# Kernel tuning notes

Hardware: AMD Instinct MI355X
Metric: run time of the kernel (lower is better)

The kernel has to match this reference:

```python
import jax, jax.numpy as jnp
import numpy as np

B, T, N = 16, 16, 1024          # patients, max visits, code_num
C, G, H, A, P = 48, 32, 150, 32, 32  # code_size, graph_size, hidden_size, t_attention_size, pool attn size
OUT = 1
NEG = -1e30


def setup_inputs() -> dict:
    key = jax.random.key(0)
    ks = jax.random.split(key, 20)
    code_x = (jax.random.uniform(ks[0], (B, T, N)) < 0.2).astype(jnp.float32)
    neighbors = (jax.random.uniform(ks[1], (B, T, N)) < 0.2).astype(jnp.float32)
    cat = jax.random.randint(ks[2], (B, T, N), 0, 8)
    # divided[..., 0/1/2] = disjoint m1 (persistent) / m2 (emerging-neighbor) / m3 (emerging-unrelated) masks
    divided = jnp.stack([(cat == 0), (cat == 1), (cat == 2)], axis=-1).astype(jnp.int32)
    lens = jax.random.randint(ks[3], (B,), 1, T + 1)
    prior = jax.random.uniform(ks[4], (N,))
    adj = (jax.random.uniform(ks[5], (N, N)) * (jax.random.uniform(ks[6], (N, N)) < 0.05)).astype(jnp.float32)

    def nrm(k, shape, scale=0.05):
        return (jax.random.normal(k, shape) * scale).astype(jnp.float32)

    return dict(
        code_x=code_x, divided=divided, neighbors=neighbors, lens=lens, prior=prior, adj=adj,
        c_emb=nrm(ks[7], (N, C)), n_emb=nrm(ks[8], (N, C)), u_emb=nrm(ks[9], (N, G)),
        Wg=nrm(ks[10], (C, G)), bg=jnp.zeros((G,), jnp.float32),
        W_ih=nrm(ks[11], (3 * H, G)), b_ih=jnp.zeros((3 * H,), jnp.float32),
        W_hh=nrm(ks[12], (3 * H, H)), b_hh=jnp.zeros((3 * H,), jnp.float32),
        Wq=nrm(ks[13], (G, A)), bq=jnp.zeros((A,), jnp.float32),
        Wk=nrm(ks[14], (G, A)), bk=jnp.zeros((A,), jnp.float32),
        Wv=nrm(ks[15], (G, H)), bv=jnp.zeros((H,), jnp.float32),
        Wp=nrm(ks[16], (H, P)), bp=jnp.zeros((P,), jnp.float32),
        ctx=nrm(ks[17], (P,)),
        Wc=nrm(ks[18], (H, OUT)), bc=jnp.zeros((OUT,), jnp.float32),
    )


def _forward(code_x, divided, neighbors, lens, prior, adj, c_emb, n_emb, u_emb,
             Wg, bg, W_ih, b_ih, W_hh, b_hh, Wq, bq, Wk, bk, Wv, bv,
             Wp, bp, ctx, Wc, bc):
    pr = prior[:, None]                                  # [N,1] disease prior scaling of graph messages
    scale = 1.0 / jnp.sqrt(jnp.asarray(A, jnp.float32))

    def gru(x, h):
        # torch nn.GRUCell semantics; x: [B,N,G], h: [B,N,H]
        gi = jnp.einsum('bng,kg->bnk', x, W_ih) + b_ih
        gh = jnp.einsum('bnh,kh->bnk', h, W_hh) + b_hh
        ir, iz, i_n = jnp.split(gi, 3, -1)
        hr, hz, h_n = jnp.split(gh, 3, -1)
        r = jax.nn.sigmoid(ir + hr)
        z = jax.nn.sigmoid(iz + hz)
        cand = jnp.tanh(i_n + r * h_n)
        return (1.0 - z) * cand + z * h

    def step(carry, xs):
        h_prev, no_prev, t = carry
        cx, nb, dv = xs                                  # [B,N], [B,N], [B,N,3]
        c = cx[..., None]
        n = nb[..., None]
        # --- GraphLayer: adjacency message passing, prior-weighted ---
        ce = c * c_emb                                   # [B,N,C]
        ne = n * n_emb
        agg_c = jnp.einsum('mn,bnc->bmc', adj, ce) * pr
        agg_n = jnp.einsum('mn,bnc->bmc', adj, ne) * pr
        co = jax.nn.leaky_relu((ce + c * (agg_c + agg_n)) @ Wg + bg)   # [B,N,G]
        no = jax.nn.leaky_relu((ne + n * (agg_n + agg_c)) @ Wg + bg)
        # --- TransitionLayer ---
        m1 = dv[..., 0] > 0
        m2 = dv[..., 1] > 0
        m3 = dv[..., 2] > 0
        m23 = m2 | m3
        h_gru = gru(co, h_prev)                          # GRU branch for persistent codes (m1)
        # attention branch: queries = prev-step neighbor embeddings (m2) or unrelated embeddings (m3)
        qf = jnp.where(m2[..., None], no_prev, 0.0) + jnp.where(m3[..., None], u_emb, 0.0)
        q = qf @ Wq + bq
        k = co @ Wk + bk
        v = co @ Wv + bv                                 # [B,N,H]
        g = jnp.einsum('bma,bna->bmn', q, k) * scale     # scores over active m2|m3 keys only
        g = jnp.where(m23[:, None, :], g, NEG)
        h_att = jnp.tanh(jnp.einsum('bmn,bnh->bmh', jax.nn.softmax(g, axis=-1), v))
        t_pos = (t > 0).astype(co.dtype)                 # m23 branch only runs for t > 0 (as in original)
        h_new = jnp.where(m1[..., None], h_gru, 0.0) + t_pos * jnp.where(m23[..., None], h_att, 0.0)
        # masked maxes (0 when the index set is empty, as in original)
        om1 = jnp.max(jnp.where(m1[..., None], h_gru, NEG), axis=1)
        om1 = jnp.where(jnp.any(m1, axis=1)[:, None], om1, 0.0)
        om23 = jnp.max(jnp.where(m23[..., None], h_att, NEG), axis=1)
        om23 = jnp.where(jnp.any(m23, axis=1)[:, None], om23, 0.0)
        out_t = om1 + t_pos * om23                       # [B,H]
        return (h_new, no, t + 1), out_t

    h0 = jnp.zeros((B, N, H), jnp.float32)
    no0 = jnp.zeros((B, N, G), jnp.float32)
    xs = (jnp.transpose(code_x, (1, 0, 2)),
          jnp.transpose(neighbors, (1, 0, 2)),
          jnp.transpose(divided, (1, 0, 2, 3)))
    _, outs = jax.lax.scan(step, (h0, no0, jnp.int32(0)), xs)
    outs = jnp.transpose(outs, (1, 0, 2))                # [B,T,H]
    # --- DotProductAttention pooling over valid (ragged) timesteps ---
    vu = (outs @ Wp + bp) @ ctx                          # [B,T]
    valid = jnp.arange(T)[None, :] < lens[:, None]
    score = jax.nn.softmax(jnp.where(valid, vu, NEG), axis=-1)
    pooled = jnp.sum(outs * score[..., None], axis=1)    # [B,H]
    # --- Classifier (dropout identity at eval, activation=None) ---
    return pooled @ Wc + bc


def reference(code_x, divided, neighbors, lens, prior, adj, c_emb, n_emb, u_emb,
              Wg, bg, W_ih, b_ih, W_hh, b_hh, Wq, bq, Wk, bk, Wv, bv,
              Wp, bp, ctx, Wc, bc):
    return _forward(code_x, divided, neighbors, lens, prior, adj, c_emb, n_emb, u_emb,
                    Wg, bg, W_ih, b_ih, W_hh, b_hh, Wq, bq, Wk, bk, Wv, bv,
                    Wp, bp, ctx, Wc, bc)
```

## Files before the change

### kernel.cpp

```cpp
#include <hip/hip_runtime.h>

#define B_ 16
#define T_ 16
#define N_ 1024
#define C_ 48
#define G_ 32
#define H_ 150
#define A_ 32
#define P_ 32
#define H3_ 450
#define NNZ_CAP 262144
#define CAP1 256
#define CAP23 384
#define CHCAP 40960
#define DCAP 256
#define SCALE_ 0.17677669529663687f

__device__ __forceinline__ unsigned fenc(float f){
  unsigned u = __float_as_uint(f);
  return (u & 0x80000000u) ? ~u : (u | 0x80000000u);
}
__device__ __forceinline__ float fdec(unsigned e){
  unsigned u = (e & 0x80000000u) ? (e & 0x7fffffffu) : ~e;
  return __uint_as_float(u);
}
__device__ __forceinline__ float sigmf(float x){ return 1.f/(1.f+__expf(-x)); }
__device__ __forceinline__ float wmaxf(float v){
  #pragma unroll
  for (int d=32; d>0; d>>=1) v = fmaxf(v, __shfl_xor(v,d));
  return v;
}

#define FMA16(W, PTR, ACC) do { \
    const float4* _c4 = (const float4*)(PTR); \
    float4 _c0=_c4[0], _c1=_c4[1], _c2=_c4[2], _c3=_c4[3]; \
    ACC[0]=fmaf((W),_c0.x,ACC[0]); ACC[1]=fmaf((W),_c0.y,ACC[1]); \
    ACC[2]=fmaf((W),_c0.z,ACC[2]); ACC[3]=fmaf((W),_c0.w,ACC[3]); \
    ACC[4]=fmaf((W),_c1.x,ACC[4]); ACC[5]=fmaf((W),_c1.y,ACC[5]); \
    ACC[6]=fmaf((W),_c1.z,ACC[6]); ACC[7]=fmaf((W),_c1.w,ACC[7]); \
    ACC[8]=fmaf((W),_c2.x,ACC[8]); ACC[9]=fmaf((W),_c2.y,ACC[9]); \
    ACC[10]=fmaf((W),_c2.z,ACC[10]); ACC[11]=fmaf((W),_c2.w,ACC[11]); \
    ACC[12]=fmaf((W),_c3.x,ACC[12]); ACC[13]=fmaf((W),_c3.y,ACC[13]); \
    ACC[14]=fmaf((W),_c3.z,ACC[14]); ACC[15]=fmaf((W),_c3.w,ACC[15]); \
  } while(0)

__global__ void k_csr_cnt(const float* __restrict__ adj, int* __restrict__ rcnt){
  int m = blockIdx.x; int tid = threadIdx.x;
  int c = 0;
  for (int n = tid; n < N_; n += 256) c += (adj[(size_t)m*N_+n] != 0.f) ? 1 : 0;
  __shared__ int sr[256];
  sr[tid]=c; __syncthreads();
  for (int s=128; s>0; s>>=1){ if (tid<s) sr[tid]+=sr[tid+s]; __syncthreads(); }
  if (tid==0) rcnt[m]=sr[0];
}
__global__ void k_csr_scan(const int* __restrict__ rcnt, int* __restrict__ rowptr){
  int lane = threadIdx.x;
  int s = 0;
  for (int r=0;r<16;++r) s += rcnt[lane*16+r];
  int incl = s;
  for (int d=1; d<64; d<<=1){ int y = __shfl_up(incl, d); if (lane>=d) incl += y; }
  int run = incl - s;
  for (int r=0;r<16;++r){ rowptr[lane*16+r] = run; run += rcnt[lane*16+r]; }
  if (lane==63) rowptr[N_] = incl;
}
__global__ void k_csr_fill(const float* __restrict__ adj, const float* __restrict__ prior,
                           const int* __restrict__ rowptr,
                           int* __restrict__ ccol, float* __restrict__ cval){
  int m = blockIdx.x; int lane = threadIdx.x;
  int base = rowptr[m];
  float pm = prior[m];
  for (int it=0; it<N_/64; ++it){
    int n = it*64+lane;
    float a = adj[(size_t)m*N_+n];
    bool pnz = (a != 0.f);
    unsigned long long mk = __ballot(pnz);
    if (pnz){
      int idx = base + __popcll(mk & ((1ULL<<lane)-1ULL));
      if (idx < NNZ_CAP){ ccol[idx]=n; cval[idx]=a*pm; }
    }
    base += __popcll(mk);
  }
}

__global__ void k_masks(const int* __restrict__ divided, int* __restrict__ lst23,
                        int* __restrict__ pos1,
                        int* __restrict__ cnt23, int* __restrict__ cnt1){
  int bt = blockIdx.x; int lane = threadIdx.x;
  int base23=0, base1=0;
  for (int it=0; it<N_/64; ++it){
    int n = it*64+lane;
    const int* dv = &divided[((size_t)bt*N_+n)*3];
    int d0=dv[0], d1=dv[1], d2=dv[2];
    bool p23 = (d1>0)||(d2>0); bool p1 = d0>0;
    unsigned long long mk23 = __ballot(p23);
    unsigned long long mk1  = __ballot(p1);
    unsigned long long ltm = (1ULL<<lane)-1ULL;
    if (p23){ int idx = base23 + __popcll(mk23 & ltm); lst23[(size_t)bt*N_+idx]=n; }
    if (p1){ int idx = base1 + __popcll(mk1 & ltm); pos1[(size_t)bt*N_+n]=idx; }
    base23 += __popcll(mk23); base1 += __popcll(mk1);
  }
  if (lane==0){ cnt23[bt]=base23; cnt1[bt]=base1; }
}

__global__ void k_chains(const int* __restrict__ divided,
                         unsigned* __restrict__ chN, int* __restrict__ nchN,
                         unsigned* __restrict__ chH, int* __restrict__ nchH,
                         unsigned* __restrict__ chLv, int* __restrict__ nLv,
                         unsigned* __restrict__ chD){
  int idx = blockIdx.x*256 + threadIdx.x;
  if (idx >= B_*N_) return;
  int b = idx >> 10, n = idx & (N_-1);
  unsigned m1m = 0;
  for (int t=0;t<T_;++t){
    int d0 = divided[(((size_t)(b*T_+t))*N_ + n)*3];
    if (d0>0) m1m |= (1u<<t);
  }
  unsigned heads = m1m & ~(m1m<<1);
  while (heads){
    int t0 = __builtin_ctz(heads); heads &= (heads-1u);
    unsigned run = m1m >> t0;
    int len = __builtin_ctz(~run);
    unsigned enc = ((unsigned)b<<18)|((unsigned)n<<8)|((unsigned)t0<<4)|(unsigned)(len-1);
    int f = 0;
    if (t0 >= 2){
      size_t pidx = ((size_t)(b*T_+t0-1)*N_ + n)*3;
      if ((divided[pidx+1] | divided[pidx+2]) > 0) f = 1;
    }
    if (f){ int i2 = atomicAdd(nchH,1); if (i2 < CHCAP) chH[i2]=enc; }
    else  { int i2 = atomicAdd(nchN,1); if (i2 < CHCAP) chN[i2]=enc; }
    if (len >= 2){ int i2 = atomicAdd(&nLv[1],1); if (i2 < 8192) chLv[i2]=enc; }
    if (len >= 3){ int i2 = atomicAdd(&nLv[2],1); if (i2 < 2048) chLv[8192+i2]=enc; }
    if (len >= 4){ int i2 = atomicAdd(&nLv[3],1); if (i2 < DCAP) chD[i2]=enc; }
  }
}

__global__ void k_wt(const float* __restrict__ W_ih, const float* __restrict__ W_hh,
                     const float* __restrict__ Wq, const float* __restrict__ bq,
                     const float* __restrict__ Wk, const float* __restrict__ Wv,
                     float* __restrict__ WihT, float* __restrict__ WhhT,
                     float* __restrict__ Md, float* __restrict__ WvT){
  int idx = blockIdx.x*256+threadIdx.x;
  if (idx < G_*H3_){ int g=idx/H3_, k=idx-g*H3_; WihT[g*H3_+k]=W_ih[(size_t)k*G_+g]; }
  int idx2 = idx - G_*H3_;
  if (idx2>=0 && idx2 < H_*H3_){ int h=idx2/H3_, k=idx2-h*H3_; WhhT[h*H3_+k]=W_hh[(size_t)k*H_+h]; }
  int e = idx - (G_*H3_ + H_*H3_);
  if (e>=0 && e<1024){
    int g=e>>5, gp=e&31;
    float acc=0.f;
    #pragma unroll
    for (int a=0;a<A_;++a) acc = fmaf(Wq[g*A_+a], Wk[gp*A_+a], acc);
    Md[e]=acc;
  }
  int e2 = e - 1024;
  if (e2>=0 && e2<32){
    float acc=0.f;
    #pragma unroll
    for (int a=0;a<A_;++a) acc = fmaf(Wk[e2*A_+a], bq[a], acc);
    Md[1024+e2]=acc;
  }
  int e3 = e - 1056;
  if (e3>=0 && e3 < H_*G_){
    int h = e3>>5, g = e3&31;
    WvT[e3] = Wv[(size_t)g*H_+h];
  }
}

__global__ void k_init(float* __restrict__ om23f, int* __restrict__ nchN,
                       int* __restrict__ nchH, int* __restrict__ nLv){
  int i = blockIdx.x*256+threadIdx.x;
  if (i<B_*T_*H_){ om23f[i]=0.f; }
  if (i==0){ *nchN = 0; *nchH = 0; }
  if (i<16) nLv[i]=0;
}

__global__ __launch_bounds__(256) void k_cono(
    const float* __restrict__ code_x, const float* __restrict__ neighbors,
    const int* __restrict__ divided,
    const int* __restrict__ rowptr, const int* __restrict__ ccol, const float* __restrict__ cval,
    const float* __restrict__ c_emb, const float* __restrict__ n_emb,
    const float* __restrict__ Wg, const float* __restrict__ bg,
    float* __restrict__ co, float* __restrict__ no_)
{
  __shared__ float sCo[4][C_], sNo[4][C_];
  int w = threadIdx.x >> 6, lane = threadIdx.x & 63;
  int gw = blockIdx.x*4 + w;
  int bt = gw >> 10, m = gw & (N_-1);
  int t = bt & (T_-1);
  const int* dv = &divided[(size_t)gw*3];
  int d0=dv[0], d1=dv[1], d2=dv[2];
  bool needCo = (d0|d1|d2) > 0;
  bool needNo = (t < T_-1) && (divided[((size_t)(gw+N_))*3+1] > 0);
  if (!needCo && !needNo) return;
  float cxm = code_x[gw], nbm = neighbors[gw];
  float acc = 0.f;
  bool needAcc = (needCo && cxm!=0.f) || (needNo && nbm!=0.f);
  if (needAcc){
    int s = rowptr[m], e = rowptr[m+1];
    if (s > NNZ_CAP) s = NNZ_CAP;
    if (e > NNZ_CAP) e = NNZ_CAP;
    int btN = bt << 10;
    for (int base = s; base < e; base += 64){
      int j = base + lane;
      int cc = 0; float wx = 0.f, wy = 0.f;
      if (j < e){
        cc = ccol[j];
        float cv = cval[j];
        float xs = code_x[btN+cc], ys = neighbors[btN+cc];
        wx = cv*xs; wy = cv*ys;
      }
      unsigned long long mk = __ballot(wx!=0.f || wy!=0.f);
      while (mk){
        int u0 = __builtin_ctzll(mk); mk &= (mk-1ULL);
        int u1 = -1;
        if (mk){ u1 = __builtin_ctzll(mk); mk &= (mk-1ULL); }
        int u1s = (u1>=0)? u1 : u0;
        int n0 = __shfl(cc,u0); float a0x=__shfl(wx,u0), a0y=__shfl(wy,u0);
        int n1 = __shfl(cc,u1s); float a1x=__shfl(wx,u1s), a1y=__shfl(wy,u1s);
        float ce0=0.f,ne0=0.f,ce1=0.f,ne1=0.f;
        if (lane < C_){
          ce0 = c_emb[(size_t)n0*C_+lane]; ne0 = n_emb[(size_t)n0*C_+lane];
          ce1 = c_emb[(size_t)n1*C_+lane]; ne1 = n_emb[(size_t)n1*C_+lane];
        }
        acc = fmaf(a0x, ce0, acc); acc = fmaf(a0y, ne0, acc);
        if (u1>=0){ acc = fmaf(a1x, ce1, acc); acc = fmaf(a1y, ne1, acc); }
      }
    }
  }
  if (lane < C_){
    sCo[w][lane] = cxm * (c_emb[(size_t)m*C_+lane] + acc);
    sNo[w][lane] = nbm * (n_emb[(size_t)m*C_+lane] + acc);
  }
  asm volatile("s_waitcnt lgkmcnt(0)" ::: "memory");
  int g = lane & 31; bool isNo = lane >= 32;
  const float* src = isNo ? sNo[w] : sCo[w];
  float a2 = bg[g];
  #pragma unroll
  for (int c=0;c<C_;++c) a2 = fmaf(src[c], Wg[c*G_+g], a2);
  float r = a2 >= 0.f ? a2 : 0.01f*a2;
  if (isNo ? needNo : needCo){
    float* dst = isNo ? no_ : co;
    dst[(size_t)gw*G_ + g] = r;
  }
}

__global__ __launch_bounds__(512) void k_attn(
    const float* __restrict__ co, const float* __restrict__ no_,
    const float* __restrict__ u_emb, const int* __restrict__ divided,
    const int* __restrict__ lst23, const int* __restrict__ cnt23, const int* __restrict__ pos1,
    const float* __restrict__ Md, const float* __restrict__ WvT, const float* __restrict__ bv,
    float* __restrict__ hsel, float* __restrict__ om23f)
{
  int b = blockIdx.x; int t = blockIdx.y + 1; int bt = b*T_ + t;
  int cnt = cnt23[bt]; if (cnt > CAP23) cnt = CAP23;
  if (cnt == 0) return;
  __shared__ int   sLst[CAP23];
  __shared__ __align__(16) float sCo[CAP23][G_];
  __shared__ float sL[CAP23];
  __shared__ unsigned sMax[H_];
  int tid = threadIdx.x;
  int grp = tid >> 8;
  int rr  = tid & 255;
  unsigned sent = fenc(-1e30f);
  for (int i=tid; i<cnt; i+=512) sLst[i] = lst23[(size_t)bt*N_+i];
  for (int i=tid; i<H_; i+=512) sMax[i] = sent;
  __syncthreads();
  for (int i=tid; i<cnt*8; i+=512){
    int rrow = i>>3, seg = i&7;
    float4 v = *(const float4*)&co[((((size_t)bt<<10) + sLst[rrow])<<5) + seg*4];
    *(float4*)&sCo[rrow][seg*4] = v;
  }
  int r0 = 2*rr, r1 = 2*rr+1;
  bool act0 = r0 < cnt, act1 = r1 < cnt;
  float qpp0[G_], qpp1[G_];
  {
    float4 qv0[8], qv1[8];
    if (act0){
      int n = sLst[r0];
      int d1 = divided[((size_t)bt*N_+n)*3+1];
      const float* qs = (d1>0) ? &no_[((((size_t)(bt-1))<<10)+n)<<5] : &u_emb[(size_t)n*G_];
      #pragma unroll
      for (int j=0;j<8;++j) qv0[j] = ((const float4*)qs)[j];
    } else {
      #pragma unroll
      for (int j=0;j<8;++j) qv0[j] = make_float4(0.f,0.f,0.f,0.f);
    }
    if (act1){
      int n = sLst[r1];
      int d1 = divided[((size_t)bt*N_+n)*3+1];
      const float* qs = (d1>0) ? &no_[((((size_t)(bt-1))<<10)+n)<<5] : &u_emb[(size_t)n*G_];
      #pragma unroll
      for (int j=0;j<8;++j) qv1[j] = ((const float4*)qs)[j];
    } else {
      #pragma unroll
      for (int j=0;j<8;++j) qv1[j] = make_float4(0.f,0.f,0.f,0.f);
    }
    #pragma unroll
    for (int j=0;j<G_;++j){ float dd = Md[1024+j]; qpp0[j]=dd; qpp1[j]=dd; }
    #pragma unroll
    for (int g=0; g<G_; ++g){
      float q0 = (g&3)==0 ? qv0[g>>2].x : (g&3)==1 ? qv0[g>>2].y : (g&3)==2 ? qv0[g>>2].z : qv0[g>>2].w;
      float q1 = (g&3)==0 ? qv1[g>>2].x : (g&3)==1 ? qv1[g>>2].y : (g&3)==2 ? qv1[g>>2].z : qv1[g>>2].w;
      const float4* mr = (const float4*)&Md[g*G_];
      #pragma unroll
      for (int j=0;j<8;++j){
        float4 mj = mr[j];
        qpp0[4*j+0]=fmaf(q0,mj.x,qpp0[4*j+0]); qpp1[4*j+0]=fmaf(q1,mj.x,qpp1[4*j+0]);
        qpp0[4*j+1]=fmaf(q0,mj.y,qpp0[4*j+1]); qpp1[4*j+1]=fmaf(q1,mj.y,qpp1[4*j+1]);
        qpp0[4*j+2]=fmaf(q0,mj.z,qpp0[4*j+2]); qpp1[4*j+2]=fmaf(q1,mj.z,qpp1[4*j+2]);
        qpp0[4*j+3]=fmaf(q0,mj.w,qpp0[4*j+3]); qpp1[4*j+3]=fmaf(q1,mj.w,qpp1[4*j+3]);
      }
    }
  }
  __syncthreads();
  int half = (cnt+1)>>1;
  int c0 = grp ? half : 0;
  int c1 = grp ? cnt  : half;
  float pb0[G_], pb1[G_]; float l0=0.f, l1=0.f;
  #pragma unroll
  for (int j=0;j<G_;++j){ pb0[j]=0.f; pb1[j]=0.f; }
  if (act0){
    for (int c=c0;c<c1;++c){
      const float4* col = (const float4*)&sCo[c][0];
      float4 xv[8];
      #pragma unroll
      for (int j=0;j<8;++j) xv[j]=col[j];
      float dA=0.f,dB=0.f,dC=0.f,dD=0.f, eA=0.f,eB=0.f,eC=0.f,eD=0.f;
      #pragma unroll
      for (int j=0;j<8;++j){
        dA = fmaf(qpp0[4*j+0], xv[j].x, dA); dB = fmaf(qpp0[4*j+1], xv[j].y, dB);
        dC = fmaf(qpp0[4*j+2], xv[j].z, dC); dD = fmaf(qpp0[4*j+3], xv[j].w, dD);
        eA = fmaf(qpp1[4*j+0], xv[j].x, eA); eB = fmaf(qpp1[4*j+1], xv[j].y, eB);
        eC = fmaf(qpp1[4*j+2], xv[j].z, eC); eD = fmaf(qpp1[4*j+3], xv[j].w, eD);
      }
      float pv0 = __expf(((dA+dB)+(dC+dD))*SCALE_);
      float pv1 = __expf(((eA+eB)+(eC+eD))*SCALE_);
      if (!act1) pv1 = 0.f;
      l0 += pv0; l1 += pv1;
      #pragma unroll
      for (int j=0;j<8;++j){
        pb0[4*j+0]=fmaf(pv0,xv[j].x,pb0[4*j+0]); pb1[4*j+0]=fmaf(pv1,xv[j].x,pb1[4*j+0]);
        pb0[4*j+1]=fmaf(pv0,xv[j].y,pb0[4*j+1]); pb1[4*j+1]=fmaf(pv1,xv[j].y,pb1[4*j+1]);
        pb0[4*j+2]=fmaf(pv0,xv[j].z,pb0[4*j+2]); pb1[4*j+2]=fmaf(pv1,xv[j].z,pb1[4*j+2]);
        pb0[4*j+3]=fmaf(pv0,xv[j].w,pb0[4*j+3]); pb1[4*j+3]=fmaf(pv1,xv[j].w,pb1[4*j+3]);
      }
    }
  }
  __syncthreads();
  if (grp==0){
    if (act0){
      #pragma unroll
      for (int j=0;j<G_;++j) sCo[r0][(j+r0)&31] = pb0[j];
      sL[r0] = l0;
    }
    if (act1){
      #pragma unroll
      for (int j=0;j<G_;++j) sCo[r1][(j+r1)&31] = pb1[j];
      sL[r1] = l1;
    }
  }
  __syncthreads();
  if (grp==1){
    if (act0){
      #pragma unroll
      for (int j=0;j<G_;++j) sCo[r0][(j+r0)&31] += pb0[j];
      sL[r0] += l0;
    }
    if (act1){
      #pragma unroll
      for (int j=0;j<G_;++j) sCo[r1][(j+r1)&31] += pb1[j];
      sL[r1] += l1;
    }
  }
  __syncthreads();
  int grp2 = tid >> 8;
  int lane = tid & 63;
  int hA = grp2*75, hB = hA + 75;
  for (int er = tid & 255; er < CAP23; er += 256){
    bool act = er < cnt;
    float pb[G_];
    if (act){
      float inv = 1.f / sL[er];
      #pragma unroll
      for (int j=0;j<G_;++j) pb[j] = sCo[er][(j+er)&31] * inv;
    } else {
      #pragma unroll
      for (int j=0;j<G_;++j) pb[j]=0.f;
    }
    bool wsel=false; float* hd=nullptr;
    if (act && t+1 < T_){
      int n = sLst[er];
      size_t nidx = ((size_t)b*T_+(t+1))*N_ + n;
      if (divided[nidx*3+0] > 0){
        int pos = pos1[nidx];
        if (pos >= 0 && pos < CAP1){ wsel=true; hd=&hsel[(((size_t)b*T_+t)*CAP1 + pos)*H_]; }
      }
    }
    for (int h=hA; h<hB; ++h){
      float acc = bv[h];
      const float4* wr = (const float4*)&WvT[h*G_];
      #pragma unroll
      for (int j=0;j<8;++j){
        float4 wj = wr[j];
        acc = fmaf(pb[4*j+0], wj.x, acc);
        acc = fmaf(pb[4*j+1], wj.y, acc);
        acc = fmaf(pb[4*j+2], wj.z, acc);
        acc = fmaf(pb[4*j+3], wj.w, acc);
      }
      float o = act ? tanhf(acc) : -1e30f;
      float om = wmaxf(o);
      if (lane==0) atomicMax(&sMax[h], fenc(om));
      if (wsel) hd[h] = o;
    }
    if (cnt <= 256) break;
  }
  __syncthreads();
  for (int i=tid; i<H_; i+=512) om23f[(size_t)bt*H_+i] = fdec(sMax[i]);
}

__global__ __launch_bounds__(256) void k_gruheadN(
    const float* __restrict__ co, const int* __restrict__ pos1,
    const unsigned* __restrict__ chN, const int* __restrict__ nchN,
    const float* __restrict__ WihT, const float* __restrict__ b_ih,
    const float* __restrict__ b_hh, float* __restrict__ gout)
{
  __shared__ __align__(16) float sCoT[G_][16];
  __shared__ float sG[16][452];
  __shared__ int sBt[16], sN[16], sPos[16];
  int tid = threadIdx.x;
  int NC = *nchN; if (NC > CHCAP) NC = CHCAP;
  int base = blockIdx.x * 16;
  if (base >= NC) return;
  int num = min(16, NC - base);
  if (tid < 16){
    if (tid < num){
      unsigned cl = chN[base+tid];
      int b = cl>>18, n = (cl>>8)&1023, t0 = (cl>>4)&15;
      int bt = b*T_ + t0;
      sBt[tid]=bt; sN[tid]=n; sPos[tid]=pos1[(size_t)bt*N_+n];
    } else { sBt[tid]=0; sN[tid]=0; sPos[tid]=-1; }
  }
  __syncthreads();
  for (int i=tid; i<G_*16; i+=256){
    int g = i>>4, ii = i&15;
    sCoT[g][ii] = (ii<num) ? co[((size_t)sBt[ii]*N_+sN[ii])*G_+g] : 0.f;
  }
  __syncthreads();
  for (int pass=0; pass<2; ++pass){
    int k = pass*256 + tid;
    if (k < H3_){
      float acc[16];
      #pragma unroll
      for (int u=0;u<16;++u) acc[u]=0.f;
      for (int g=0; g<G_; ++g){
        float wih = WihT[g*H3_ + k];
        FMA16(wih, &sCoT[g][0], acc);
      }
      #pragma unroll
      for (int u=0;u<16;++u) sG[u][k] = acc[u];
    }
  }
  __syncthreads();
  for (int i=tid; i<num*152; i+=256){
    int s = i/152, h = i - s*152;
    if (h < H_){
      int pos = sPos[s];
      if (pos >= 0 && pos < CAP1){
        float r = sigmf(sG[s][h]       + b_ih[h]       + b_hh[h]);
        float z = sigmf(sG[s][h+H_]    + b_ih[h+H_]    + b_hh[h+H_]);
        float cand = tanhf(sG[s][h+2*H_] + b_ih[h+2*H_] + r*b_hh[h+2*H_]);
        gout[((size_t)sBt[s]*CAP1 + pos)*H_ + h] = (1.f-z)*cand;
      }
    }
  }
}

__global__ __launch_bounds__(256) void k_gruheadH(
    const float* __restrict__ co, const float* __restrict__ hsel,
    const int* __restrict__ pos1,
    const unsigned* __restrict__ chH, const int* __restrict__ nchH,
    const float* __restrict__ WihT, const float* __restrict__ b_ih,
    const float* __restrict__ WhhT, const float* __restrict__ b_hh,
    float* __restrict__ gout)
{
  __shared__ __align__(16) float sCoT[G_][16];
  __shared__ __align__(16) float sHT[152][16];
  __shared__ float sG[16][452];
  __shared__ float sGhn[16][152];
  __shared__ int sBt[16], sN[16], sPos[16], sHo[16];
  int tid = threadIdx.x;
  int NC = *nchH; if (NC > CHCAP) NC = CHCAP;
  int base = blockIdx.x * 16;
  if (base >= NC) return;
  int num = min(16, NC - base);
  if (tid < 16){
    if (tid < num){
      unsigned cl = chH[base+tid];
      int b = cl>>18, n = (cl>>8)&1023, t0 = (cl>>4)&15;
      int bt = b*T_ + t0;
      int pos = pos1[(size_t)bt*N_+n];
      sBt[tid]=bt; sN[tid]=n; sPos[tid]=pos;
      sHo[tid] = (b*T_ + (t0-1))*CAP1 + ((pos>=0 && pos<CAP1) ? pos : 0);
    } else { sBt[tid]=0; sN[tid]=0; sPos[tid]=-1; sHo[tid]=0; }
  }
  __syncthreads();
  for (int i=tid; i<G_*16; i+=256){
    int g = i>>4, ii = i&15;
    sCoT[g][ii] = (ii<num) ? co[((size_t)sBt[ii]*N_+sN[ii])*G_+g] : 0.f;
  }
  for (int i=tid; i<152*16; i+=256){
    int q = i>>4, ii = i&15;
    float v = 0.f;
    if (ii < num && q < H_) v = hsel[(size_t)sHo[ii]*H_ + q];
    sHT[q][ii] = v;
  }
  __syncthreads();
  for (int pass=0; pass<2; ++pass){
    int k = pass*256 + tid;
    if (k < H3_){
      float acc[16];
      #pragma unroll
      for (int u=0;u<16;++u) acc[u]=0.f;
      for (int g=0; g<G_; ++g){
        float wih = WihT[g*H3_ + k];
        FMA16(wih, &sCoT[g][0], acc);
      }
      #pragma unroll
      for (int u=0;u<16;++u) sG[u][k] = acc[u];
    }
  }
  for (int pass=0; pass<2; ++pass){
    int k = pass*256 + tid;
    if (k < H3_){
      float acc[16];
      #pragma unroll
      for (int u=0;u<16;++u) acc[u]=0.f;
      for (int q=0; q<H_; ++q){
        float whh = WhhT[q*H3_ + k];
        FMA16(whh, &sHT[q][0], acc);
      }
      if (k < 2*H_){
        #pragma unroll
        for (int u=0;u<16;++u) sG[u][k] += acc[u];
      } else {
        #pragma unroll
        for (int u=0;u<16;++u) sGhn[u][k-2*H_] = acc[u];
      }
    }
  }
  __syncthreads();
  for (int i=tid; i<num*152; i+=256){
    int s = i/152, h = i - s*152;
    if (h < H_){
      int pos = sPos[s];
      if (pos >= 0 && pos < CAP1){
        float hv = sHT[h][s];
        float r = sigmf(sG[s][h]       + b_ih[h]       + b_hh[h]);
        float z = sigmf(sG[s][h+H_]    + b_ih[h+H_]    + b_hh[h+H_]);
        float cand = tanhf(sG[s][h+2*H_] + b_ih[h+2*H_] + r*(sGhn[s][h] + b_hh[h+2*H_]));
        float o = (1.f-z)*cand + z*hv;
        gout[((size_t)sBt[s]*CAP1 + pos)*H_ + h] = o;
      }
    }
  }
}

__global__ __launch_bounds__(256) void k_grulev(
    const float* __restrict__ co, const int* __restrict__ pos1,
    const unsigned* __restrict__ chLv, const int* __restrict__ nLv,
    const float* __restrict__ WihT, const float* __restrict__ b_ih,
    const float* __restrict__ WhhT, const float* __restrict__ b_hh,
    float* __restrict__ gout, int s, int cap)
{
  __shared__ __align__(16) float sCoT[G_][16];
  __shared__ __align__(16) float sHT[152][16];
  __shared__ float sG[16][452];
  __shared__ float sGhn[16][152];
  __shared__ int sBt[16], sN[16], sPos[16], sHo[16];
  int tid = threadIdx.x;
  int NC = *nLv; if (NC > cap) NC = cap;
  int base = blockIdx.x * 16;
  if (base >= NC) return;
  int num = min(16, NC - base);
  if (tid < 16){
    if (tid < num){
      unsigned cl = chLv[base+tid];
      int b = cl>>18, n = (cl>>8)&1023, t0 = (cl>>4)&15;
      int bt = b*T_ + t0 + s;
      int pos = pos1[(size_t)bt*N_+n];
      int posp = pos1[(size_t)(bt-1)*N_+n];
      if (posp < 0 || posp >= CAP1) posp = 0;
      sBt[tid]=bt; sN[tid]=n; sPos[tid]=pos;
      sHo[tid] = (bt-1)*CAP1 + posp;
    } else { sBt[tid]=0; sN[tid]=0; sPos[tid]=-1; sHo[tid]=0; }
  }
  __syncthreads();
  for (int i=tid; i<G_*16; i+=256){
    int g = i>>4, ii = i&15;
    sCoT[g][ii] = (ii<num) ? co[((size_t)sBt[ii]*N_+sN[ii])*G_+g] : 0.f;
  }
  for (int i=tid; i<152*16; i+=256){
    int q = i>>4, ii = i&15;
    float v = 0.f;
    if (ii < num && q < H_) v = gout[(size_t)sHo[ii]*H_ + q];
    sHT[q][ii] = v;
  }
  __syncthreads();
  for (int pass=0; pass<2; ++pass){
    int k = pass*256 + tid;
    if (k < H3_){
      float acc[16];
      #pragma unroll
      for (int u=0;u<16;++u) acc[u]=0.f;
      for (int g=0; g<G_; ++g){
        float wih = WihT[g*H3_ + k];
        FMA16(wih, &sCoT[g][0], acc);
      }
      #pragma unroll
      for (int u=0;u<16;++u) sG[u][k] = acc[u];
    }
  }
  for (int pass=0; pass<2; ++pass){
    int k = pass*256 + tid;
    if (k < H3_){
      float acc[16];
      #pragma unroll
      for (int u=0;u<16;++u) acc[u]=0.f;
      for (int q=0; q<H_; ++q){
        float whh = WhhT[q*H3_ + k];
        FMA16(whh, &sHT[q][0], acc);
      }
      if (k < 2*H_){
        #pragma unroll
        for (int u=0;u<16;++u) sG[u][k] += acc[u];
      } else {
        #pragma unroll
        for (int u=0;u<16;++u) sGhn[u][k-2*H_] = acc[u];
      }
    }
  }
  __syncthreads();
  for (int i=tid; i<num*152; i+=256){
    int sl = i/152, h = i - sl*152;
    if (h < H_){
      int pos = sPos[sl];
      if (pos >= 0 && pos < CAP1){
        float hv = sHT[h][sl];
        float r = sigmf(sG[sl][h]       + b_ih[h]       + b_hh[h]);
        float z = sigmf(sG[sl][h+H_]    + b_ih[h+H_]    + b_hh[h+H_]);
        float cand = tanhf(sG[sl][h+2*H_] + b_ih[h+2*H_] + r*(sGhn[sl][h] + b_hh[h+2*H_]));
        float o = (1.f-z)*cand + z*hv;
        gout[((size_t)sBt[sl]*CAP1 + pos)*H_ + h] = o;
      }
    }
  }
}

__global__ __launch_bounds__(256) void k_grudeep(
    const float* __restrict__ co, const int* __restrict__ pos1,
    const unsigned* __restrict__ chD, const int* __restrict__ nD,
    const float* __restrict__ WihT, const float* __restrict__ b_ih,
    const float* __restrict__ WhhT, const float* __restrict__ b_hh,
    float* __restrict__ gout)
{
  __shared__ float hst[4][4][H_];
  int w = threadIdx.x >> 6, lane = threadIdx.x & 63;
  int NC = *nD; if (NC > DCAP) NC = DCAP;
  if (NC == 0) return;
  int cbase = (blockIdx.x*4 + w)*4;
  if (cbase >= NC) return;

  int cbv[4], cnv[4], t0v[4], lenv[4];
  #pragma unroll
  for (int u=0;u<4;++u){
    int cid = cbase+u; bool ca = cid < NC;
    unsigned cl = chD[ca ? cid : (NC-1)];
    cbv[u]=cl>>18; cnv[u]=(cl>>8)&1023; t0v[u]=(cl>>4)&15;
    lenv[u]= ca ? (int)((cl&15)+1) : 3;
  }
  int maxlen = lenv[0];
  #pragma unroll
  for (int u=1;u<4;++u) maxlen = max(maxlen, lenv[u]);

  int h0=lane,h1=lane+64,h2=lane+128; bool has2=(h2<H_); int h2c=has2?h2:0;
  float bi[9], bh[9];
  bi[0]=b_ih[h0]; bi[1]=b_ih[h0+H_]; bi[2]=b_ih[h0+2*H_];
  bi[3]=b_ih[h1]; bi[4]=b_ih[h1+H_]; bi[5]=b_ih[h1+2*H_];
  bi[6]=b_ih[h2c]; bi[7]=b_ih[h2c+H_]; bi[8]=b_ih[h2c+2*H_];
  bh[0]=b_hh[h0]; bh[1]=b_hh[h0+H_]; bh[2]=b_hh[h0+2*H_];
  bh[3]=b_hh[h1]; bh[4]=b_hh[h1+H_]; bh[5]=b_hh[h1+2*H_];
  bh[6]=b_hh[h2c]; bh[7]=b_hh[h2c+H_]; bh[8]=b_hh[h2c+2*H_];

  for (int s=3; s<maxlen; ++s){
    bool as[4]; int btv[4];
    const float* hp[4];
    #pragma unroll
    for (int u=0;u<4;++u){
      as[u] = s < lenv[u];
      int t = t0v[u] + (as[u] ? s : 0);
      btv[u] = cbv[u]*T_ + t;
      if (s == 3 && as[u]){
        int btp = btv[u] - 1;
        int posp = pos1[(size_t)btp*N_ + cnv[u]];
        if (posp < 0 || posp >= CAP1) posp = 0;
        hp[u] = &gout[((size_t)btp*CAP1 + posp)*H_];
      } else {
        hp[u] = &hst[w][u][0];
      }
    }
    float gi[4][9], gh[4][9];
    #pragma unroll
    for (int u=0;u<4;++u){
      #pragma unroll
      for (int j=0;j<9;++j){ gi[u][j]=bi[j]; gh[u][j]=bh[j]; }
    }
    const float* cop[4];
    #pragma unroll
    for (int u=0;u<4;++u) cop[u] = &co[((size_t)btv[u]*N_ + cnv[u])*G_];
    for (int g=0; g<G_; ++g){
      const float* wr = &WihT[g*H3_];
      float wv[9];
      wv[0]=wr[h0]; wv[1]=wr[h0+H_]; wv[2]=wr[h0+2*H_];
      wv[3]=wr[h1]; wv[4]=wr[h1+H_]; wv[5]=wr[h1+2*H_];
      wv[6]=wr[h2c]; wv[7]=wr[h2c+H_]; wv[8]=wr[h2c+2*H_];
      #pragma unroll
      for (int u=0;u<4;++u){
        float cg = cop[u][g];
        #pragma unroll
        for (int j=0;j<9;++j) gi[u][j]=fmaf(cg, wv[j], gi[u][j]);
      }
    }
    for (int q=0;q<H_;++q){
      const float* wr=&WhhT[q*H3_];
      float wv[9];
      wv[0]=wr[h0]; wv[1]=wr[h0+H_]; wv[2]=wr[h0+2*H_];
      wv[3]=wr[h1]; wv[4]=wr[h1+H_]; wv[5]=wr[h1+2*H_];
      wv[6]=wr[h2c]; wv[7]=wr[h2c+H_]; wv[8]=wr[h2c+2*H_];
      #pragma unroll
      for (int u=0;u<4;++u){
        float hv = hp[u][q];
        #pragma unroll
        for (int j=0;j<9;++j) gh[u][j]=fmaf(hv, wv[j], gh[u][j]);
      }
    }
    #pragma unroll
    for (int u=0;u<4;++u){
      if (as[u]){
        float hv0 = hp[u][h0];
        float hv1 = hp[u][h1];
        float hv2 = has2 ? hp[u][h2] : 0.f;
        float r0=sigmf(gi[u][0]+gh[u][0]), z0=sigmf(gi[u][1]+gh[u][1]);
        float cd0=tanhf(gi[u][2]+r0*gh[u][2]);
        float o0=(1.f-z0)*cd0 + z0*hv0;
        float r1=sigmf(gi[u][3]+gh[u][3]), z1=sigmf(gi[u][4]+gh[u][4]);
        float cd1=tanhf(gi[u][5]+r1*gh[u][5]);
        float o1=(1.f-z1)*cd1 + z1*hv1;
        float o2=0.f;
        if (has2){
          float r2=sigmf(gi[u][6]+gh[u][6]), z2=sigmf(gi[u][7]+gh[u][7]);
          float cd2=tanhf(gi[u][8]+r2*gh[u][8]);
          o2=(1.f-z2)*cd2 + z2*hv2;
        }
        float* hd = &hst[w][u][0];
        hd[h0]=o0; hd[h1]=o1; if (has2) hd[h2]=o2;
        int pos = pos1[(size_t)btv[u]*N_ + cnv[u]];
        if (pos >= 0 && pos < CAP1){
          float* gd = &gout[((size_t)btv[u]*CAP1 + pos)*H_];
          gd[h0]=o0; gd[h1]=o1; if (has2) gd[h2]=o2;
        }
      }
    }
    asm volatile("s_waitcnt lgkmcnt(0)" ::: "memory");
  }
}

__global__ __launch_bounds__(256) void k_om1(
    const float* __restrict__ gout, const int* __restrict__ cnt1, float* __restrict__ om1f)
{
  int bt = blockIdx.x; int tid = threadIdx.x;
  int c1 = cnt1[bt]; if (c1 > CAP1) c1 = CAP1;
  if (tid < H_){
    float mx = -1e30f;
    for (int r=0;r<c1;++r) mx = fmaxf(mx, gout[((size_t)bt*CAP1+r)*H_+tid]);
    om1f[(size_t)bt*H_+tid] = (c1>0) ? mx : 0.f;
  }
}

__global__ __launch_bounds__(256) void k_final(
    const float* __restrict__ om1f, const float* __restrict__ om23f,
    const float* __restrict__ Wp, const float* __restrict__ bp,
    const float* __restrict__ ctx, const float* __restrict__ Wc, const float* __restrict__ bc,
    const int* __restrict__ lens, float* __restrict__ out)
{
  int b = blockIdx.x; int tid = threadIdx.x;
  __shared__ float sOut[T_][H_];
  __shared__ float sTP[T_][P_];
  __shared__ float sVu[T_], sSc[T_], sPool[H_];
  __shared__ float sRed[256];
  for (int i=tid; i<T_*H_; i+=256){
    int t=i/H_, h=i-t*H_;
    float o1 = om1f[((size_t)b*T_+t)*H_+h];
    float o2 = (t>0)? om23f[((size_t)b*T_+t)*H_+h] : 0.f;
    sOut[t][h]=o1+o2;
  }
  __syncthreads();
  for (int pr = tid; pr < T_*P_; pr += 256){
    int t = pr / P_, p = pr - t*P_;
    float acc = bp[p];
    for (int h=0;h<H_;++h) acc = fmaf(sOut[t][h], Wp[h*P_+p], acc);
    sTP[t][p] = acc * ctx[p];
  }
  __syncthreads();
  if (tid < T_){
    float v=0.f;
    for (int p=0;p<P_;++p) v += sTP[tid][p];
    sVu[tid]=v;
  }
  __syncthreads();
  if (tid==0){
    int L = lens[b]; if (L<1) L=1; if (L>T_) L=T_;
    float mx=-1e30f;
    for (int t=0;t<L;++t) mx = fmaxf(mx, sVu[t]);
    float s=0.f;
    for (int t=0;t<L;++t){ float e=__expf(sVu[t]-mx); sSc[t]=e; s+=e; }
    float inv=1.f/s;
    for (int t=0;t<T_;++t) sSc[t] = (t<L)? sSc[t]*inv : 0.f;
  }
  __syncthreads();
  if (tid < H_){
    float acc=0.f;
    for (int t=0;t<T_;++t) acc = fmaf(sOut[t][tid], sSc[t], acc);
    sPool[tid]=acc;
  }
  __syncthreads();
  float v = (tid<H_)? sPool[tid]*Wc[tid] : 0.f;
  sRed[tid]=v; __syncthreads();
  for (int s=128;s>0;s>>=1){ if (tid<s) sRed[tid]+=sRed[tid+s]; __syncthreads(); }
  if (tid==0) out[b] = sRed[0] + bc[0];
}

extern "C" void kernel_launch(void* const* d_in, const int* in_sizes, int n_in,
                              void* d_out, int out_size, void* d_ws, size_t ws_size,
                              hipStream_t stream)
{
  const float* code_x=(const float*)d_in[0];
  const int*   divided=(const int*)d_in[1];
  const float* neighbors=(const float*)d_in[2];
  const int*   lens=(const int*)d_in[3];
  const float* prior=(const float*)d_in[4];
  const float* adj=(const float*)d_in[5];
  const float* c_emb=(const float*)d_in[6];
  const float* n_emb=(const float*)d_in[7];
  const float* u_emb=(const float*)d_in[8];
  const float* Wg=(const float*)d_in[9];
  const float* bg=(const float*)d_in[10];
  const float* W_ih=(const float*)d_in[11];
  const float* b_ih=(const float*)d_in[12];
  const float* W_hh=(const float*)d_in[13];
  const float* b_hh=(const float*)d_in[14];
  const float* Wq=(const float*)d_in[15];
  const float* bq=(const float*)d_in[16];
  const float* Wk=(const float*)d_in[17];
  const float* bk=(const float*)d_in[18];
  const float* Wv=(const float*)d_in[19];
  const float* bv=(const float*)d_in[20];
  const float* Wp=(const float*)d_in[21];
  const float* bp=(const float*)d_in[22];
  const float* ctx=(const float*)d_in[23];
  const float* Wc=(const float*)d_in[24];
  const float* bc=(const float*)d_in[25];
  float* out=(float*)d_out;
  (void)in_sizes; (void)n_in; (void)out_size; (void)ws_size; (void)bk;

  char* p=(char*)d_ws;
  size_t off=0;
  auto carve=[&](size_t bytes)->char*{ char* r=p+off; off=(off+bytes+255)&~(size_t)255; return r; };
  int*   rowptr=(int*)carve((N_+1)*4);
  int*   rcnt  =(int*)carve(N_*4);
  int*   ccol  =(int*)carve((size_t)NNZ_CAP*4);
  float* cval  =(float*)carve((size_t)NNZ_CAP*4);
  int*   cnt23 =(int*)carve(B_*T_*4);
  int*   cnt1  =(int*)carve(B_*T_*4);
  int*   lst23 =(int*)carve((size_t)B_*T_*N_*4);
  int*   pos1  =(int*)carve((size_t)B_*T_*N_*4);
  float* co    =(float*)carve((size_t)B_*T_*N_*G_*4);
  float* no_   =(float*)carve((size_t)B_*T_*N_*G_*4);
  float* WihT  =(float*)carve((size_t)G_*H3_*4);
  float* WhhT  =(float*)carve((size_t)H_*H3_*4);
  float* Md    =(float*)carve(1056*4);
  float* WvT   =(float*)carve((size_t)H_*G_*4);
  float* hsel  =(float*)carve((size_t)B_*T_*CAP1*H_*4);
  float* gout  =(float*)carve((size_t)B_*T_*CAP1*H_*4);
  unsigned* chainsN=(unsigned*)carve((size_t)CHCAP*4);
  unsigned* chainsH=(unsigned*)carve((size_t)CHCAP*4);
  unsigned* chLv  =(unsigned*)carve((size_t)10240*4);
  unsigned* chD   =(unsigned*)carve((size_t)DCAP*4);
  int*   nchN  =(int*)carve(256);
  int*   nchH  =(int*)carve(256);
  int*   nLv   =(int*)carve(256);
  float* om1f  =(float*)carve((size_t)B_*T_*H_*4);
  float* om23f =(float*)carve((size_t)B_*T_*H_*4);

  k_csr_cnt<<<N_,256,0,stream>>>(adj, rcnt);
  k_csr_scan<<<1,64,0,stream>>>(rcnt, rowptr);
  k_csr_fill<<<N_,64,0,stream>>>(adj, prior, rowptr, ccol, cval);
  k_masks<<<B_*T_,64,0,stream>>>(divided, lst23, pos1, cnt23, cnt1);
  k_wt<<<343,256,0,stream>>>(W_ih, W_hh, Wq, bq, Wk, Wv, WihT, WhhT, Md, WvT);
  k_init<<<(B_*T_*H_+255)/256,256,0,stream>>>(om23f, nchN, nchH, nLv);
  k_chains<<<(B_*N_+255)/256,256,0,stream>>>(divided, chainsN, nchN, chainsH, nchH, chLv, nLv, chD);
  k_cono<<<B_*T_*N_/4,256,0,stream>>>(code_x, neighbors, divided, rowptr, ccol, cval,
                                      c_emb, n_emb, Wg, bg, co, no_);
  k_attn<<<dim3(B_, T_-1),512,0,stream>>>(co, no_, u_emb, divided,
                                      lst23, cnt23, pos1, Md, WvT, bv,
                                      hsel, om23f);
  k_gruheadN<<<CHCAP/16,256,0,stream>>>(co, pos1, chainsN, nchN,
                                      WihT, b_ih, b_hh, gout);
  k_gruheadH<<<CHCAP/16,256,0,stream>>>(co, hsel, pos1, chainsH, nchH,
                                      WihT, b_ih, WhhT, b_hh, gout);
  k_grulev<<<512,256,0,stream>>>(co, pos1, chLv, nLv+1,
                                      WihT, b_ih, WhhT, b_hh, gout, 1, 8192);
  k_grulev<<<128,256,0,stream>>>(co, pos1, chLv+8192, nLv+2,
                                      WihT, b_ih, WhhT, b_hh, gout, 2, 2048);
  k_grudeep<<<DCAP/16,256,0,stream>>>(co, pos1, chD, nLv+3,
                                      WihT, b_ih, WhhT, b_hh, gout);
  k_om1<<<B_*T_,256,0,stream>>>(gout, cnt1, om1f);
  k_final<<<B_,256,0,stream>>>(om1f, om23f, Wp,bp,ctx,Wc,bc, lens, out);
}
```

Before: 530.6 us.

## Widen attention block to 768 threads and split key range four ways

The attention kernel now launches 768 threads per (patient, visit) block instead of 512. The key loop is split across four thread groups of 192 instead of two of 256, with their partial sums reduced in shared memory over four synchronised rounds. The value projection stage now maps each of up to 384 rows to its own thread, so the 256-row second pass is gone. The goal is more parallelism in a kernel launched on only 240 blocks, at the cost of more register pressure under the larger launch bound and extra barriers.

Measured after the change: 803.4 us. +51.4%, slower.

```diff
diff --git a/kernel.cpp b/kernel.cpp
--- a/kernel.cpp
+++ b/kernel.cpp
@@ -243,7 +243,7 @@
   }
 }
 
-__global__ __launch_bounds__(512) void k_attn(
+__global__ __launch_bounds__(768) void k_attn(
     const float* __restrict__ co, const float* __restrict__ no_,
     const float* __restrict__ u_emb, const int* __restrict__ divided,
     const int* __restrict__ lst23, const int* __restrict__ cnt23, const int* __restrict__ pos1,
@@ -258,19 +258,19 @@
   __shared__ float sL[CAP23];
   __shared__ unsigned sMax[H_];
   int tid = threadIdx.x;
-  int grp = tid >> 8;
-  int rr  = tid & 255;
+  int grp = tid / 192;
+  int rr  = tid - grp*192;
+  int r0 = 2*rr, r1 = 2*rr+1;
+  bool act0 = r0 < cnt, act1 = r1 < cnt;
   unsigned sent = fenc(-1e30f);
-  for (int i=tid; i<cnt; i+=512) sLst[i] = lst23[(size_t)bt*N_+i];
-  for (int i=tid; i<H_; i+=512) sMax[i] = sent;
-  __syncthreads();
-  for (int i=tid; i<cnt*8; i+=512){
+  for (int i=tid; i<cnt; i+=768) sLst[i] = lst23[(size_t)bt*N_+i];
+  for (int i=tid; i<H_; i+=768) sMax[i] = sent;
+  __syncthreads();
+  for (int i=tid; i<cnt*8; i+=768){
     int rrow = i>>3, seg = i&7;
     float4 v = *(const float4*)&co[((((size_t)bt<<10) + sLst[rrow])<<5) + seg*4];
     *(float4*)&sCo[rrow][seg*4] = v;
   }
-  int r0 = 2*rr, r1 = 2*rr+1;
-  bool act0 = r0 < cnt, act1 = r1 < cnt;
   float qpp0[G_], qpp1[G_];
   {
     float4 qv0[8], qv1[8];
@@ -312,13 +312,14 @@
     }
   }
   __syncthreads();
-  int half = (cnt+1)>>1;
-  int c0 = grp ? half : 0;
-  int c1 = grp ? cnt  : half;
+  int quart = (cnt+3)>>2;
+  int c0 = grp*quart;
+  int c1 = c0 + quart; if (c1 > cnt) c1 = cnt;
   float pb0[G_], pb1[G_]; float l0=0.f, l1=0.f;
   #pragma unroll
   for (int j=0;j<G_;++j){ pb0[j]=0.f; pb1[j]=0.f; }
   if (act0){
+    #pragma unroll 2
     for (int c=c0;c<c1;++c){
       const float4* col = (const float4*)&sCo[c][0];
       float4 xv[8];
@@ -333,8 +334,7 @@
         eC = fmaf(qpp1[4*j+2], xv[j].z, eC); eD = fmaf(qpp1[4*j+3], xv[j].w, eD);
       }
       float pv0 = __expf(((dA+dB)+(dC+dD))*SCALE_);
-      float pv1 = __expf(((eA+eB)+(eC+eD))*SCALE_);
-      if (!act1) pv1 = 0.f;
+      float pv1 = act1 ? __expf(((eA+eB)+(eC+eD))*SCALE_) : 0.f;
       l0 += pv0; l1 += pv1;
       #pragma unroll
       for (int j=0;j<8;++j){
@@ -346,75 +346,75 @@
     }
   }
   __syncthreads();
-  if (grp==0){
-    if (act0){
-      #pragma unroll
-      for (int j=0;j<G_;++j) sCo[r0][(j+r0)&31] = pb0[j];
-      sL[r0] = l0;
-    }
-    if (act1){
-      #pragma unroll
-      for (int j=0;j<G_;++j) sCo[r1][(j+r1)&31] = pb1[j];
-      sL[r1] = l1;
-    }
-  }
-  __syncthreads();
-  if (grp==1){
-    if (act0){
-      #pragma unroll
-      for (int j=0;j<G_;++j) sCo[r0][(j+r0)&31] += pb0[j];
-      sL[r0] += l0;
-    }
-    if (act1){
-      #pragma unroll
-      for (int j=0;j<G_;++j) sCo[r1][(j+r1)&31] += pb1[j];
-      sL[r1] += l1;
-    }
-  }
-  __syncthreads();
-  int grp2 = tid >> 8;
+  #pragma unroll
+  for (int g=0; g<4; ++g){
+    if (grp == g){
+      if (act0){
+        if (g == 0){
+          #pragma unroll
+          for (int j=0;j<G_;++j) sCo[r0][(j+r0)&31] = pb0[j];
+          sL[r0] = l0;
+        } else {
+          #pragma unroll
+          for (int j=0;j<G_;++j) sCo[r0][(j+r0)&31] += pb0[j];
+          sL[r0] += l0;
+        }
+      }
+      if (act1){
+        if (g == 0){
+          #pragma unroll
+          for (int j=0;j<G_;++j) sCo[r1][(j+r1)&31] = pb1[j];
+          sL[r1] = l1;
+        } else {
+          #pragma unroll
+          for (int j=0;j<G_;++j) sCo[r1][(j+r1)&31] += pb1[j];
+          sL[r1] += l1;
+        }
+      }
+    }
+    __syncthreads();
+  }
+  int grp2 = (tid >= 384) ? 1 : 0;
+  int er   = tid - 384*grp2;
   int lane = tid & 63;
+  bool act = (er < cnt);
+  float pb[G_];
+  if (act){
+    float inv = 1.f / sL[er];
+    #pragma unroll
+    for (int j=0;j<G_;++j) pb[j] = sCo[er][(j+er)&31] * inv;
+  } else {
+    #pragma unroll
+    for (int j=0;j<G_;++j) pb[j]=0.f;
+  }
+  bool wsel=false; float* hd=nullptr;
+  if (act && t+1 < T_){
+    int n = sLst[er];
+    size_t nidx = ((size_t)b*T_+(t+1))*N_ + n;
+    if (divided[nidx*3+0] > 0){
+      int pos = pos1[nidx];
+      if (pos >= 0 && pos < CAP1){ wsel=true; hd=&hsel[(((size_t)b*T_+t)*CAP1 + pos)*H_]; }
+    }
+  }
   int hA = grp2*75, hB = hA + 75;
-  for (int er = tid & 255; er < CAP23; er += 256){
-    bool act = er < cnt;
-    float pb[G_];
-    if (act){
-      float inv = 1.f / sL[er];
-      #pragma unroll
-      for (int j=0;j<G_;++j) pb[j] = sCo[er][(j+er)&31] * inv;
-    } else {
-      #pragma unroll
-      for (int j=0;j<G_;++j) pb[j]=0.f;
-    }
-    bool wsel=false; float* hd=nullptr;
-    if (act && t+1 < T_){
-      int n = sLst[er];
-      size_t nidx = ((size_t)b*T_+(t+1))*N_ + n;
-      if (divided[nidx*3+0] > 0){
-        int pos = pos1[nidx];
-        if (pos >= 0 && pos < CAP1){ wsel=true; hd=&hsel[(((size_t)b*T_+t)*CAP1 + pos)*H_]; }
-      }
-    }
-    for (int h=hA; h<hB; ++h){
-      float acc = bv[h];
-      const float4* wr = (const float4*)&WvT[h*G_];
-      #pragma unroll
-      for (int j=0;j<8;++j){
-        float4 wj = wr[j];
-        acc = fmaf(pb[4*j+0], wj.x, acc);
-        acc = fmaf(pb[4*j+1], wj.y, acc);
-        acc = fmaf(pb[4*j+2], wj.z, acc);
-        acc = fmaf(pb[4*j+3], wj.w, acc);
-      }
-      float o = act ? tanhf(acc) : -1e30f;
-      float om = wmaxf(o);
-      if (lane==0) atomicMax(&sMax[h], fenc(om));
-      if (wsel) hd[h] = o;
-    }
-    if (cnt <= 256) break;
-  }
-  __syncthreads();
-  for (int i=tid; i<H_; i+=512) om23f[(size_t)bt*H_+i] = fdec(sMax[i]);
+  for (int h=hA; h<hB; ++h){
+    float acc = bv[h];
+    const float4* wr = (const float4*)&WvT[h*G_];
+    #pragma unroll
+    for (int j=0;j<8;++j){
+      float4 wj = wr[j];
+      acc = fmaf(pb[4*j+0], wj.x, acc);
+      acc = fmaf(pb[4*j+1], wj.y, acc);
+      acc = fmaf(pb[4*j+2], wj.z, acc);
+      acc = fmaf(pb[4*j+3], wj.w, acc);
+    }
+    float o = act ? tanhf(acc) : -1e30f;
+    float om = wmaxf(o);
+    if (lane==0) atomicMax(&sMax[h], fenc(om));
+    if (wsel) hd[h] = o;
+  }
+  __syncthreads();
+  for (int i=tid; i<H_; i+=768) om23f[(size_t)bt*H_+i] = fdec(sMax[i]);
 }
 
 __global__ __launch_bounds__(256) void k_gruheadN(
@@ -909,7 +909,7 @@
   k_chains<<<(B_*N_+255)/256,256,0,stream>>>(divided, chainsN, nchN, chainsH, nchH, chLv, nLv, chD);
   k_cono<<<B_*T_*N_/4,256,0,stream>>>(code_x, neighbors, divided, rowptr, ccol, cval,
                                       c_emb, n_emb, Wg, bg, co, no_);
-  k_attn<<<dim3(B_, T_-1),512,0,stream>>>(co, no_, u_emb, divided,
+  k_attn<<<dim3(B_, T_-1),768,0,stream>>>(co, no_, u_emb, divided,
                                       lst23, cnt23, pos1, Md, WvT, bv,
                                       hsel, om23f);
   k_gruheadN<<<CHCAP/16,256,0,stream>>>(co, pos1, chainsN, nchN,
```
